# Kernel tuning notes

Hardware: AMD Instinct MI355X
Metric: run time of the kernel (lower is better)

Reference implementation:

```python
import jax, jax.numpy as jnp
import numpy as np
from jax import lax
from jax.scipy.special import logsumexp

NUM_BINS = 1001          # num_bins
K = 127                  # num_quantized_bins = 2**(8-1) - 1 (signed int8, non-narrow)
HALF = NUM_BINS // 2     # 500
EPS = 1e-4               # smoothing_eps
NEG = -1e30              # mask value for logsumexp


def setup_inputs() -> dict:
    key = jax.random.key(0)
    x = jax.random.normal(key, (8, 4096, 1024), dtype=jnp.float32)
    return {"x": x}


def _smooth_logits(v, valid, L):
    # Faithful to smooth_normalize_distribution: hist += eps*is_zeros - eps1*n_nonzeros
    is_zero = valid & (v == 0)
    n_zeros = jnp.sum(is_zero).astype(jnp.float32)
    n_nz = L.astype(jnp.float32) - n_zeros
    eps1 = EPS * n_zeros / jnp.maximum(n_nz, 1.0)
    logits = v + EPS * is_zero.astype(jnp.float32) - eps1 * n_nz
    return logits, n_nz


def reference(x):
    absmax = jnp.max(jnp.abs(x))
    edges = jnp.linspace(-absmax, absmax, NUM_BINS + 1)           # hist_edges, len 1002
    counts, _ = jnp.histogram(x.ravel(), bins=edges)
    hist = lax.stop_gradient(counts.astype(jnp.float32))          # torch.histc(...).int()
    csum = jnp.concatenate([jnp.zeros(1, jnp.float32), jnp.cumsum(hist)])  # exclusive prefix
    total = csum[-1]
    hist_pad = jnp.concatenate([hist, jnp.zeros(NUM_BINS, jnp.float32)])
    k = jnp.arange(NUM_BINS)

    def per_candidate(i):
        start = HALF - i
        stop = HALF + i + 1
        L = 2 * i + 1                          # length of sliced histogram
        valid = k < L
        sliced = lax.dynamic_slice(hist_pad, (start,), (NUM_BINS,))  # first L entries valid
        left = csum[start]                     # sum(hist[:start])
        right = total - csum[stop]             # sum(hist[stop:])
        p = sliced.at[0].add(left).at[L - 1].add(right)
        m = L // K                             # num_merged_bins
        seg = jnp.minimum(k // m, K - 1)       # merged-bin id per position (remainder -> last)
        seg_v = jnp.where(valid, seg, K)       # dump invalid into extra segment
        qb = jax.ops.segment_sum(jnp.where(valid, sliced, 0.0), seg_v, num_segments=K + 1)[:K]
        nz = valid & (sliced != 0)
        # norm for bin j counts nonzeros in its range; last bin uses stop=-1 (excludes k=L-1)
        cnt_mask = nz & (k != L - 1)
        norms = jax.ops.segment_sum(cnt_mask.astype(jnp.float32), seg_v, num_segments=K + 1)[:K]
        nk = norms[seg]
        qbk = qb[seg]
        # q[start:stop] = qb[j]/norm where norm != 0; k=L-1 never assigned; q[sliced==0]=0
        q = jnp.where(nz & (k != L - 1) & (nk > 0), qbk / jnp.maximum(nk, 1.0), 0.0)

        p_log, _ = _smooth_logits(p, valid, L)
        q_log, n_nz_q = _smooth_logits(q, valid, L)
        lZp = logsumexp(jnp.where(valid, p_log, NEG))
        lZq = logsumexp(jnp.where(valid, q_log, NEG))
        lp = p_log - lZp
        lq = q_log - lZq
        probs = jnp.where(valid, jnp.exp(lp), 0.0)
        kl = jnp.sum(probs * (lp - lq) * valid)
        kl = jnp.where(n_nz_q > 0, kl, jnp.inf)  # q all-zero -> divergence = inf
        return edges[stop], kl

    ivals = jnp.arange(K // 2, HALF + 1)        # i = 63 .. 500 (438 candidates)
    thresholds, divergence = jax.vmap(per_candidate)(ivals)
    return thresholds[jnp.argmin(divergence)]
```

## Files before the change

### kernel.cpp

```cpp
#include <hip/hip_runtime.h>
#include <math.h>

#define NBINS 1001
#define KQ 127
#define HALFB 500
#define SEPS 1e-4f
#define NCAND 438
#define IMIN 63


static __device__ __forceinline__ float edge_at(int j, float stepv, float negabs) {
    return __fadd_rn(__fmul_rn((float)j, stepv), negabs);
}

static __device__ __forceinline__ void blockSum2(double& a, double& b, double* s8) {
    for (int s = 32; s > 0; s >>= 1) {
        a += __shfl_down(a, s, 64);
        b += __shfl_down(b, s, 64);
    }
    const int w = threadIdx.x >> 6, l = threadIdx.x & 63;
    __syncthreads();
    if (l == 0) { s8[w] = a; s8[4 + w] = b; }
    __syncthreads();
    a = (s8[0] + s8[1]) + (s8[2] + s8[3]);
    b = (s8[4] + s8[5]) + (s8[6] + s8[7]);
}

static __device__ __forceinline__ double blockSum1(double a, double* s8) {
    for (int s = 32; s > 0; s >>= 1) a += __shfl_down(a, s, 64);
    const int w = threadIdx.x >> 6, l = threadIdx.x & 63;
    __syncthreads();
    if (l == 0) s8[w] = a;
    __syncthreads();
    return (s8[0] + s8[1]) + (s8[2] + s8[3]);
}

static __device__ __forceinline__ float blockMaxF(float a, double* s8) {
    for (int s = 32; s > 0; s >>= 1) a = fmaxf(a, __shfl_down(a, s, 64));
    const int w = threadIdx.x >> 6, l = threadIdx.x & 63;
    __syncthreads();
    if (l == 0) s8[w] = (double)a;
    __syncthreads();
    return fmaxf(fmaxf((float)s8[0], (float)s8[1]), fmaxf((float)s8[2], (float)s8[3]));
}


__global__ void init_kernel(unsigned int* ws_u) {
    int t = threadIdx.x;
    if (t == 0) ws_u[0] = 0u;
    if (t < NBINS) ws_u[4 + t] = 0u;
}

__global__ __launch_bounds__(256) void absmax_kernel(const float* __restrict__ x,
                                                     long long n,
                                                     unsigned int* absmax_bits) {
    __shared__ float red[256];
    float m = 0.f;
    long long idx = (long long)blockIdx.x * blockDim.x + threadIdx.x;
    long long stride = (long long)gridDim.x * blockDim.x;
    const float4* x4 = (const float4*)x;
    long long n4 = n >> 2;
    for (long long i = idx; i < n4; i += stride) {
        float4 v = x4[i];
        m = fmaxf(m, fmaxf(fmaxf(fabsf(v.x), fabsf(v.y)), fmaxf(fabsf(v.z), fabsf(v.w))));
    }
    for (long long i = (n4 << 2) + idx; i < n; i += stride)
        m = fmaxf(m, fabsf(x[i]));
    red[threadIdx.x] = m;
    __syncthreads();
    for (int s = 128; s > 0; s >>= 1) {
        if (threadIdx.x < s) red[threadIdx.x] = fmaxf(red[threadIdx.x], red[threadIdx.x + s]);
        __syncthreads();
    }
    if (threadIdx.x == 0) atomicMax(absmax_bits, __float_as_uint(red[0]));
}

static __device__ __forceinline__ void bin_one(float v, float inv, float cofs,
                                               float stepv, float negabs,
                                               unsigned int* __restrict__ sh) {
    float t = __builtin_fmaf(v, inv, cofs);
    int b = (int)t;
    b = b < 0 ? 0 : (b > NBINS - 1 ? NBINS - 1 : b);
    float e_lo = edge_at(b, stepv, negabs);
    float e_hi = edge_at(b + 1, stepv, negabs);
    int up = (v >= e_hi) & (b < NBINS - 1);
    int dn = (v < e_lo) & (b > 0);
    b += up - dn;
    atomicAdd(&sh[b], 1u);
}

__global__ __launch_bounds__(256) void hist_kernel(const float* __restrict__ x,
                                                   long long n,
                                                   const unsigned int* __restrict__ absmax_bits,
                                                   unsigned int* __restrict__ hist) {
    __shared__ unsigned int sh[4 * NBINS];
    for (int i = threadIdx.x; i < 4 * NBINS; i += blockDim.x) sh[i] = 0u;
    __syncthreads();
    unsigned int* mysh = sh + (threadIdx.x >> 6) * NBINS;

    float absmax = __uint_as_float(*absmax_bits);
    float negabs = -absmax;
    float stepv = __fdiv_rn(__fmul_rn(2.0f, absmax), 1001.0f);
    float inv = __fdiv_rn(1001.0f, __fmul_rn(2.0f, absmax));
    float cofs = __fmul_rn(absmax, inv);

    long long idx = (long long)blockIdx.x * blockDim.x + threadIdx.x;
    long long stride = (long long)gridDim.x * blockDim.x;
    const float4* x4 = (const float4*)x;
    long long n4 = n >> 2;
    for (long long i = idx; i < n4; i += stride) {
        float4 v = x4[i];
        bin_one(v.x, inv, cofs, stepv, negabs, mysh);
        bin_one(v.y, inv, cofs, stepv, negabs, mysh);
        bin_one(v.z, inv, cofs, stepv, negabs, mysh);
        bin_one(v.w, inv, cofs, stepv, negabs, mysh);
    }
    for (long long i = (n4 << 2) + idx; i < n; i += stride)
        bin_one(x[i], inv, cofs, stepv, negabs, mysh);

    __syncthreads();
    for (int i = threadIdx.x; i < NBINS; i += blockDim.x) {
        unsigned int s = sh[i] + sh[NBINS + i] + sh[2 * NBINS + i] + sh[3 * NBINS + i];
        if (s) atomicAdd(&hist[i], s);
    }
}

__global__ __launch_bounds__(256) void cand_kernel(const unsigned int* __restrict__ hist,
                                                   float* __restrict__ divg) {
    const int i = IMIN + (int)blockIdx.x;
    const int L = 2 * i + 1;
    const int start = HALFB - i;
    const int stop = start + L;
    const int m = L / KQ;
    const int tid = threadIdx.x;

    __shared__ float s_h[NBINS];
    __shared__ float s_qb[KQ];
    __shared__ int s_norm[KQ];
    __shared__ double s8[8];

    for (int k = tid; k < NBINS; k += 256) s_h[k] = (float)hist[k];
    if (tid < KQ) { s_qb[tid] = 0.f; s_norm[tid] = 0; }
    __syncthreads();

    double lsum = 0.0, rsum = 0.0;
    for (int k = tid; k < start; k += 256) lsum += (double)s_h[k];
    for (int k = stop + tid; k < NBINS; k += 256) rsum += (double)s_h[k];
    blockSum2(lsum, rsum, s8);
    float left = (float)lsum, right = (float)rsum;

    float sl[4], ppre[4];
    float zp = 0.f;
    float maxppre = -INFINITY;
#pragma unroll
    for (int j = 0; j < 4; ++j) {
        int k = tid + 256 * j;
        sl[j] = 0.f; ppre[j] = 0.f;
        if (k < L) {
            float s = s_h[start + k];
            sl[j] = s;
            int seg = k / m; if (seg > KQ - 1) seg = KQ - 1;
            atomicAdd(&s_qb[seg], s);
            if (s != 0.f && k != L - 1) atomicAdd(&s_norm[seg], 1);
            float p = s;
            if (k == 0) p += left;
            if (k == L - 1) p += right;
            float pp = (p == 0.f) ? SEPS : p;
            ppre[j] = pp;
            if (p == 0.f) zp += 1.f;
            maxppre = fmaxf(maxppre, pp);
        }
    }
    __syncthreads();

    double zpd = (double)zp;
    double nnzd = (tid < KQ) ? (double)s_norm[tid] : 0.0;
    blockSum2(zpd, nnzd, s8);
    float n_zeros_p = (float)zpd;
    int nnzq = (int)nnzd;
    float maxp = blockMaxF(maxppre, s8);

    float n_nz_p = (float)L - n_zeros_p;
    float eps1p = SEPS * n_zeros_p / fmaxf(n_nz_p, 1.0f);
    float cp = eps1p * n_nz_p;

    float n_zeros_q = (float)L - (float)nnzq;
    float n_nz_qf = (float)L - n_zeros_q;
    float eps1q = SEPS * n_zeros_q / fmaxf(n_nz_qf, 1.0f);
    float cq = eps1q * n_nz_qf;

    float qpre[4];
    float maxqpre = -INFINITY;
#pragma unroll
    for (int j = 0; j < 4; ++j) {
        int k = tid + 256 * j;
        qpre[j] = 0.f;
        if (k < L) {
            float s = sl[j];
            int seg = k / m; if (seg > KQ - 1) seg = KQ - 1;
            float qv = 0.f;
            int nk = s_norm[seg];
            if (s != 0.f && k != L - 1 && nk > 0) qv = s_qb[seg] / (float)nk;
            float qq = (qv == 0.f) ? SEPS : qv;
            qpre[j] = qq;
            maxqpre = fmaxf(maxqpre, qq);
        }
    }
    float maxq = blockMaxF(maxqpre, s8);
    float maxplog = maxp - cp;
    float maxqlog = maxq - cq;

    double sp = 0.0, sq = 0.0;
#pragma unroll
    for (int j = 0; j < 4; ++j) {
        int k = tid + 256 * j;
        if (k < L) {
            sp += (double)expf((ppre[j] - cp) - maxplog);
            sq += (double)expf((qpre[j] - cq) - maxqlog);
        }
    }
    blockSum2(sp, sq, s8);
    float lZp = maxplog + (float)log(sp);
    float lZq = maxqlog + (float)log(sq);

    double kll = 0.0;
#pragma unroll
    for (int j = 0; j < 4; ++j) {
        int k = tid + 256 * j;
        if (k < L) {
            float pl = ppre[j] - cp;
            float ql = qpre[j] - cq;
            float lp = pl - lZp;
            float lq = ql - lZq;
            kll += (double)(expf(lp) * (lp - lq));
        }
    }
    double KL = blockSum1(kll, s8);
    if (tid == 0) divg[blockIdx.x] = (nnzq > 0) ? (float)KL : INFINITY;
}

__global__ void argmin_kernel(const float* __restrict__ divg,
                              const unsigned int* __restrict__ absmax_bits,
                              float* __restrict__ out) {
    __shared__ float vals[512];
    __shared__ int idxs[512];
    int tid = threadIdx.x;
    vals[tid] = (tid < NCAND) ? divg[tid] : INFINITY;
    idxs[tid] = tid;
    __syncthreads();
    for (int s = 256; s > 0; s >>= 1) {
        if (tid < s) {
            float a = vals[tid], b = vals[tid + s];
            int ia = idxs[tid], ib = idxs[tid + s];
            if (b < a || (b == a && ib < ia)) { vals[tid] = b; idxs[tid] = ib; }
        }
        __syncthreads();
    }
    if (tid == 0) {
        int i = IMIN + idxs[0];
        int stop = HALFB + i + 1;
        float absmax = __uint_as_float(*absmax_bits);
        float stepv = __fdiv_rn(__fmul_rn(2.0f, absmax), 1001.0f);
        out[0] = __fadd_rn(__fmul_rn((float)stop, stepv), -absmax);
    }
}

extern "C" void kernel_launch(void* const* d_in, const int* in_sizes, int n_in,
                              void* d_out, int out_size, void* d_ws, size_t ws_size,
                              hipStream_t stream) {
    const float* x = (const float*)d_in[0];
    long long n = (long long)in_sizes[0];

    unsigned int* ws_u = (unsigned int*)d_ws;
    unsigned int* absmax_bits = ws_u;
    unsigned int* hist = ws_u + 4;
    float* divg = (float*)(ws_u + 1028);
    float* out = (float*)d_out;

    hipLaunchKernelGGL(init_kernel, dim3(1), dim3(1024), 0, stream, ws_u);
    hipLaunchKernelGGL(absmax_kernel, dim3(2048), dim3(256), 0, stream, x, n, absmax_bits);
    hipLaunchKernelGGL(hist_kernel, dim3(1024), dim3(256), 0, stream, x, n, absmax_bits, hist);
    hipLaunchKernelGGL(cand_kernel, dim3(NCAND), dim3(256), 0, stream, hist, divg);
    hipLaunchKernelGGL(argmin_kernel, dim3(1), dim3(512), 0, stream, divg, absmax_bits, out);
}
```

Before: 258.1 us.

## Precompute histogram prefix sums and replace per-candidate atomics with scan lookups

Adds a single-block scan kernel that builds double prefix sums of the histogram and prefix counts of nonzero bins. Each candidate block then reads left/right tail sums, merged-bin sums and nonzero counts directly instead of using shared-memory atomics and several block reductions, and fuses the two max reductions into one. The absmax and histogram loops are also unrolled by two to put more loads in flight. The cost is an extra kernel launch and small changes in summation order that could shift floating-point results.

```diff
diff --git a/kernel.cpp b/kernel.cpp
--- a/kernel.cpp
+++ b/kernel.cpp
@@ -35,13 +35,17 @@
     return (s8[0] + s8[1]) + (s8[2] + s8[3]);
 }
 
-static __device__ __forceinline__ float blockMaxF(float a, double* s8) {
-    for (int s = 32; s > 0; s >>= 1) a = fmaxf(a, __shfl_down(a, s, 64));
+static __device__ __forceinline__ void blockMax2(float& a, float& b, double* s8) {
+    for (int s = 32; s > 0; s >>= 1) {
+        a = fmaxf(a, __shfl_down(a, s, 64));
+        b = fmaxf(b, __shfl_down(b, s, 64));
+    }
     const int w = threadIdx.x >> 6, l = threadIdx.x & 63;
     __syncthreads();
-    if (l == 0) s8[w] = (double)a;
-    __syncthreads();
-    return fmaxf(fmaxf((float)s8[0], (float)s8[1]), fmaxf((float)s8[2], (float)s8[3]));
+    if (l == 0) { s8[w] = (double)a; s8[4 + w] = (double)b; }
+    __syncthreads();
+    a = fmaxf(fmaxf((float)s8[0], (float)s8[1]), fmaxf((float)s8[2], (float)s8[3]));
+    b = fmaxf(fmaxf((float)s8[4], (float)s8[5]), fmaxf((float)s8[6], (float)s8[7]));
 }
 
 
@@ -60,12 +64,19 @@
     long long stride = (long long)gridDim.x * blockDim.x;
     const float4* x4 = (const float4*)x;
     long long n4 = n >> 2;
-    for (long long i = idx; i < n4; i += stride) {
-        float4 v = x4[i];
-        m = fmaxf(m, fmaxf(fmaxf(fabsf(v.x), fabsf(v.y)), fmaxf(fabsf(v.z), fabsf(v.w))));
-    }
-    for (long long i = (n4 << 2) + idx; i < n; i += stride)
-        m = fmaxf(m, fabsf(x[i]));
+    long long i = idx;
+    for (; i + stride < n4; i += 2 * stride) {
+        float4 a = x4[i];
+        float4 b = x4[i + stride];
+        m = fmaxf(m, fmaxf(fmaxf(fabsf(a.x), fabsf(a.y)), fmaxf(fabsf(a.z), fabsf(a.w))));
+        m = fmaxf(m, fmaxf(fmaxf(fabsf(b.x), fabsf(b.y)), fmaxf(fabsf(b.z), fabsf(b.w))));
+    }
+    for (; i < n4; i += stride) {
+        float4 a = x4[i];
+        m = fmaxf(m, fmaxf(fmaxf(fabsf(a.x), fabsf(a.y)), fmaxf(fabsf(a.z), fabsf(a.w))));
+    }
+    for (long long j = (n4 << 2) + idx; j < n; j += stride)
+        m = fmaxf(m, fabsf(x[j]));
     red[threadIdx.x] = m;
     __syncthreads();
     for (int s = 128; s > 0; s >>= 1) {
@@ -108,107 +119,134 @@
     long long stride = (long long)gridDim.x * blockDim.x;
     const float4* x4 = (const float4*)x;
     long long n4 = n >> 2;
-    for (long long i = idx; i < n4; i += stride) {
-        float4 v = x4[i];
-        bin_one(v.x, inv, cofs, stepv, negabs, mysh);
-        bin_one(v.y, inv, cofs, stepv, negabs, mysh);
-        bin_one(v.z, inv, cofs, stepv, negabs, mysh);
-        bin_one(v.w, inv, cofs, stepv, negabs, mysh);
-    }
-    for (long long i = (n4 << 2) + idx; i < n; i += stride)
-        bin_one(x[i], inv, cofs, stepv, negabs, mysh);
-
-    __syncthreads();
-    for (int i = threadIdx.x; i < NBINS; i += blockDim.x) {
-        unsigned int s = sh[i] + sh[NBINS + i] + sh[2 * NBINS + i] + sh[3 * NBINS + i];
-        if (s) atomicAdd(&hist[i], s);
-    }
+    long long i = idx;
+    for (; i + stride < n4; i += 2 * stride) {
+        float4 a = x4[i];
+        float4 b = x4[i + stride];
+        bin_one(a.x, inv, cofs, stepv, negabs, mysh);
+        bin_one(a.y, inv, cofs, stepv, negabs, mysh);
+        bin_one(a.z, inv, cofs, stepv, negabs, mysh);
+        bin_one(a.w, inv, cofs, stepv, negabs, mysh);
+        bin_one(b.x, inv, cofs, stepv, negabs, mysh);
+        bin_one(b.y, inv, cofs, stepv, negabs, mysh);
+        bin_one(b.z, inv, cofs, stepv, negabs, mysh);
+        bin_one(b.w, inv, cofs, stepv, negabs, mysh);
+    }
+    for (; i < n4; i += stride) {
+        float4 a = x4[i];
+        bin_one(a.x, inv, cofs, stepv, negabs, mysh);
+        bin_one(a.y, inv, cofs, stepv, negabs, mysh);
+        bin_one(a.z, inv, cofs, stepv, negabs, mysh);
+        bin_one(a.w, inv, cofs, stepv, negabs, mysh);
+    }
+    for (long long j = (n4 << 2) + idx; j < n; j += stride)
+        bin_one(x[j], inv, cofs, stepv, negabs, mysh);
+
+    __syncthreads();
+    for (int i2 = threadIdx.x; i2 < NBINS; i2 += blockDim.x) {
+        unsigned int s = sh[i2] + sh[NBINS + i2] + sh[2 * NBINS + i2] + sh[3 * NBINS + i2];
+        if (s) atomicAdd(&hist[i2], s);
+    }
+}
+
+__global__ __launch_bounds__(1024) void scan_kernel(const unsigned int* __restrict__ hist,
+                                                    double* __restrict__ csumD,
+                                                    int* __restrict__ nzc) {
+    __shared__ double sd[1024];
+    __shared__ int si[1024];
+    int t = threadIdx.x;
+    unsigned int h = (t < NBINS) ? hist[t] : 0u;
+    sd[t] = (double)((float)h);
+    si[t] = (t < NBINS && h != 0u) ? 1 : 0;
+    __syncthreads();
+    for (int off = 1; off < 1024; off <<= 1) {
+        double dv = 0.0; int iv = 0;
+        if (t >= off) { dv = sd[t - off]; iv = si[t - off]; }
+        __syncthreads();
+        sd[t] += dv; si[t] += iv;
+        __syncthreads();
+    }
+    if (t < NBINS) { csumD[t + 1] = sd[t]; nzc[t + 1] = si[t]; }
+    if (t == 0) { csumD[0] = 0.0; nzc[0] = 0; }
 }
 
 __global__ __launch_bounds__(256) void cand_kernel(const unsigned int* __restrict__ hist,
+                                                   const double* __restrict__ csumD,
+                                                   const int* __restrict__ nzc,
                                                    float* __restrict__ divg) {
     const int i = IMIN + (int)blockIdx.x;
     const int L = 2 * i + 1;
     const int start = HALFB - i;
     const int stop = start + L;
     const int m = L / KQ;
+    const unsigned int magic = (65536u + (unsigned)m - 1u) / (unsigned)m;
     const int tid = threadIdx.x;
 
     __shared__ float s_h[NBINS];
     __shared__ float s_qb[KQ];
-    __shared__ int s_norm[KQ];
+    __shared__ float s_nkf[KQ];
     __shared__ double s8[8];
 
     for (int k = tid; k < NBINS; k += 256) s_h[k] = (float)hist[k];
-    if (tid < KQ) { s_qb[tid] = 0.f; s_norm[tid] = 0; }
-    __syncthreads();
-
-    double lsum = 0.0, rsum = 0.0;
-    for (int k = tid; k < start; k += 256) lsum += (double)s_h[k];
-    for (int k = stop + tid; k < NBINS; k += 256) rsum += (double)s_h[k];
-    blockSum2(lsum, rsum, s8);
-    float left = (float)lsum, right = (float)rsum;
-
-    float sl[4], ppre[4];
-    float zp = 0.f;
-    float maxppre = -INFINITY;
+
+    double csS = csumD[start], csE = csumD[stop], total = csumD[NBINS];
+    float left = (float)csS;
+    float right = (float)(total - csE);
+    float s0 = (float)hist[start];
+    float sL1 = (float)hist[stop - 1];
+    int nzwin = nzc[stop] - nzc[start];
+    int nnzq = nzwin - ((sL1 != 0.f) ? 1 : 0);
+    int nzeros_s = L - nzwin;
+    float n_zeros_p = (float)(nzeros_s
+                              - ((s0 == 0.f && csS > 0.0) ? 1 : 0)
+                              - ((sL1 == 0.f && (total - csE) > 0.0) ? 1 : 0));
+
+    float n_nz_p = (float)L - n_zeros_p;
+    float eps1p = SEPS * n_zeros_p / fmaxf(n_nz_p, 1.0f);
+    float cp = eps1p * n_nz_p;
+
+    float n_zeros_q = (float)L - (float)nnzq;
+    float n_nz_qf = (float)L - n_zeros_q;
+    float eps1q = SEPS * n_zeros_q / fmaxf(n_nz_qf, 1.0f);
+    float cq = eps1q * n_nz_qf;
+
+    if (tid < KQ) {
+        int lo = start + tid * m;
+        int hi = (tid == KQ - 1) ? stop : (lo + m);
+        s_qb[tid] = (float)(csumD[hi] - csumD[lo]);
+        int nrm = (nzc[hi] - nzc[lo]) - ((tid == KQ - 1 && sL1 != 0.f) ? 1 : 0);
+        s_nkf[tid] = (float)nrm;
+    }
+    __syncthreads();
+
+    float ppre[4], qpre[4];
+    float maxpp = -INFINITY, maxqq = -INFINITY;
 #pragma unroll
     for (int j = 0; j < 4; ++j) {
         int k = tid + 256 * j;
-        sl[j] = 0.f; ppre[j] = 0.f;
+        ppre[j] = 0.f; qpre[j] = 0.f;
         if (k < L) {
             float s = s_h[start + k];
-            sl[j] = s;
-            int seg = k / m; if (seg > KQ - 1) seg = KQ - 1;
-            atomicAdd(&s_qb[seg], s);
-            if (s != 0.f && k != L - 1) atomicAdd(&s_norm[seg], 1);
             float p = s;
             if (k == 0) p += left;
             if (k == L - 1) p += right;
             float pp = (p == 0.f) ? SEPS : p;
-            ppre[j] = pp;
-            if (p == 0.f) zp += 1.f;
-            maxppre = fmaxf(maxppre, pp);
+            int seg = (int)(((unsigned)k * magic) >> 16);
+            if (seg > KQ - 1) seg = KQ - 1;
+            float qv = 0.f;
+            if (s != 0.f && k != L - 1) {
+                float nk = s_nkf[seg];
+                if (nk > 0.f) qv = s_qb[seg] / nk;
+            }
+            float qq = (qv == 0.f) ? SEPS : qv;
+            ppre[j] = pp; qpre[j] = qq;
+            maxpp = fmaxf(maxpp, pp);
+            maxqq = fmaxf(maxqq, qq);
         }
     }
-    __syncthreads();
-
-    double zpd = (double)zp;
-    double nnzd = (tid < KQ) ? (double)s_norm[tid] : 0.0;
-    blockSum2(zpd, nnzd, s8);
-    float n_zeros_p = (float)zpd;
-    int nnzq = (int)nnzd;
-    float maxp = blockMaxF(maxppre, s8);
-
-    float n_nz_p = (float)L - n_zeros_p;
-    float eps1p = SEPS * n_zeros_p / fmaxf(n_nz_p, 1.0f);
-    float cp = eps1p * n_nz_p;
-
-    float n_zeros_q = (float)L - (float)nnzq;
-    float n_nz_qf = (float)L - n_zeros_q;
-    float eps1q = SEPS * n_zeros_q / fmaxf(n_nz_qf, 1.0f);
-    float cq = eps1q * n_nz_qf;
-
-    float qpre[4];
-    float maxqpre = -INFINITY;
-#pragma unroll
-    for (int j = 0; j < 4; ++j) {
-        int k = tid + 256 * j;
-        qpre[j] = 0.f;
-        if (k < L) {
-            float s = sl[j];
-            int seg = k / m; if (seg > KQ - 1) seg = KQ - 1;
-            float qv = 0.f;
-            int nk = s_norm[seg];
-            if (s != 0.f && k != L - 1 && nk > 0) qv = s_qb[seg] / (float)nk;
-            float qq = (qv == 0.f) ? SEPS : qv;
-            qpre[j] = qq;
-            maxqpre = fmaxf(maxqpre, qq);
-        }
-    }
-    float maxq = blockMaxF(maxqpre, s8);
-    float maxplog = maxp - cp;
-    float maxqlog = maxq - cq;
+    blockMax2(maxpp, maxqq, s8);
+    float maxplog = maxpp - cp;
+    float maxqlog = maxqq - cq;
 
     double sp = 0.0, sq = 0.0;
 #pragma unroll
@@ -275,11 +313,14 @@
     unsigned int* absmax_bits = ws_u;
     unsigned int* hist = ws_u + 4;
     float* divg = (float*)(ws_u + 1028);
+    double* csumD = (double*)(ws_u + 1536);
+    int* nzc = (int*)(ws_u + 3544);
     float* out = (float*)d_out;
 
     hipLaunchKernelGGL(init_kernel, dim3(1), dim3(1024), 0, stream, ws_u);
     hipLaunchKernelGGL(absmax_kernel, dim3(2048), dim3(256), 0, stream, x, n, absmax_bits);
     hipLaunchKernelGGL(hist_kernel, dim3(1024), dim3(256), 0, stream, x, n, absmax_bits, hist);
-    hipLaunchKernelGGL(cand_kernel, dim3(NCAND), dim3(256), 0, stream, hist, divg);
+    hipLaunchKernelGGL(scan_kernel, dim3(1), dim3(1024), 0, stream, hist, csumD, nzc);
+    hipLaunchKernelGGL(cand_kernel, dim3(NCAND), dim3(256), 0, stream, hist, csumD, nzc, divg);
     hipLaunchKernelGGL(argmin_kernel, dim3(1), dim3(512), 0, stream, divg, absmax_bits, out);
 }
```

Result: no change. 256.5 us (-0.6%).
